# Kernel optimization log

Measured on AMD Instinct MI355X. Metric: run time of the kernel, lower is better.

## Reference

```python
import jax, jax.numpy as jnp
import numpy as np

B, N, D_IN, D_OUT, E = 16, 16384, 128, 128, 65536
LN_EPS = 1e-5


def setup_inputs() -> dict:
    key = jax.random.key(0)
    k1, k2, k3, k4 = jax.random.split(key, 4)
    x = jax.random.normal(k1, (B, N, D_IN), dtype=jnp.float32)
    edge_index = jax.random.randint(k2, (2, E), 0, N, dtype=jnp.int64)
    W_self = jax.random.normal(k3, (D_OUT, D_IN), dtype=jnp.float32) / np.sqrt(D_IN)
    W_neigh = jax.random.normal(k4, (D_OUT, D_IN), dtype=jnp.float32) / np.sqrt(D_IN)
    return {
        "x": x,
        "edge_index": edge_index,
        "batch_size": B,
        "W_self": W_self,
        "W_neigh": W_neigh,
        "bias": jnp.zeros((D_OUT,), jnp.float32),
        "gamma": jnp.ones((D_OUT,), jnp.float32),
        "beta": jnp.zeros((D_OUT,), jnp.float32),
    }


def reference(x, edge_index, batch_size, W_self, W_neigh, bias, gamma, beta):
    b, n, d = x.shape
    src, dst = edge_index[0], edge_index[1]
    # expand edge index for disjoint batched graphs: add per-graph node offsets
    offsets = (jnp.arange(batch_size, dtype=src.dtype) * n)[:, None]  # [B,1]
    src_e = (src[None, :] + offsets).reshape(-1)  # [B*E]
    dst_e = (dst[None, :] + offsets).reshape(-1)
    x_flat = x.reshape(batch_size * n, d)
    # scatter-sum neighbor features and degrees, then mean
    agg = jax.ops.segment_sum(x_flat[src_e], dst_e, num_segments=batch_size * n)
    deg = jax.ops.segment_sum(jnp.ones_like(dst_e, dtype=x_flat.dtype), dst_e,
                              num_segments=batch_size * n)
    neigh = agg / jnp.maximum(deg, 1.0)[:, None]
    out = x_flat @ W_self.T + neigh @ W_neigh.T + bias  # [B*N, D_OUT]
    # LayerNorm over last dim
    mu = jnp.mean(out, axis=-1, keepdims=True)
    var = jnp.mean(jnp.square(out - mu), axis=-1, keepdims=True)
    out = (out - mu) * jax.lax.rsqrt(var + LN_EPS) * gamma + beta
    out = jax.nn.relu(out)
    return out.reshape(batch_size, n, -1)
```

## Files before the change

kernel.cpp:

```cpp
#include <hip/hip_runtime.h>
#include <hip/hip_bf16.h>
#include <stdint.h>

#define B_ 16
#define N_ 16384
#define D_ 128
#define E_ 65536

typedef __attribute__((ext_vector_type(8))) __bf16 bf16x8;
typedef __attribute__((ext_vector_type(4))) float f32x4;
typedef __attribute__((ext_vector_type(4))) _Float16 half4;
typedef __attribute__((ext_vector_type(8))) _Float16 half8;

__device__ __forceinline__ uint16_t f2bf(float f) {
    union { float f; uint32_t u; } v;
    v.f = f;
    uint32_t u = v.u;
    uint32_t r = (u + 0x7fffu + ((u >> 16) & 1u)) >> 16;
    return (uint16_t)r;
}

__device__ __forceinline__ int As_off(int ch, int l16) {
    int c = (ch & 7) ^ ((l16 >> 4) & 1);
    return ch * 1024 + ((l16 ^ c) << 4);
}

__device__ __forceinline__ bool ei_is64(const int* __restrict__ ei, int t) {
    int w = ei[2 * (t & 63) + 1];
    return __ballot(w != 0) == 0ull;
}

__global__ void k_cntpack(const int* __restrict__ ei,
                          const float* __restrict__ wself,
                          const float* __restrict__ wneigh,
                          const float* __restrict__ x,
                          int* __restrict__ deg,
                          uint16_t* __restrict__ wpack,
                          _Float16* __restrict__ xh) {
    int t = threadIdx.x;
    int bid = blockIdx.x;
    if (bid < 256) {
        bool is64 = ei_is64(ei, t);
        int e = bid * 256 + t;
        int d = is64 ? ei[2 * (E_ + e)] : ei[E_ + e];
        atomicAdd(&deg[d], 1);
    } else if (bid < 384) {
        int g = (bid - 256) * 256 + t;
        int j = g & 7;
        int lane = (g >> 3) & 63;
        int nt = (g >> 9) & 7;
        int ks = g >> 12;
        int k = ks * 32 + (lane >> 4) * 8 + j;
        int n = nt * 16 + (lane & 15);
        float v = (k < 128) ? wself[n * 128 + k] : wneigh[n * 128 + (k - 128)];
        wpack[g] = f2bf(v);
    } else {
        size_t base = (size_t)(bid - 384) * 8192 + (size_t)t * 8;
#pragma unroll
        for (int it = 0; it < 4; it++) {
            size_t idx = base + (size_t)it * 2048;
            const float4* p = (const float4*)(x + idx);
            float4 v0 = p[0], v1 = p[1];
            union { _Float16 hh[8]; uint4 u; } pk;
            pk.hh[0] = (_Float16)v0.x; pk.hh[1] = (_Float16)v0.y;
            pk.hh[2] = (_Float16)v0.z; pk.hh[3] = (_Float16)v0.w;
            pk.hh[4] = (_Float16)v1.x; pk.hh[5] = (_Float16)v1.y;
            pk.hh[6] = (_Float16)v1.z; pk.hh[7] = (_Float16)v1.w;
            *(uint4*)(xh + idx) = pk.u;
        }
    }
}

__global__ void k_scan(const int* __restrict__ deg, int* __restrict__ off,
                       int* __restrict__ cur) {
    __shared__ int ps[256];
    int t = threadIdx.x;
    int vals[64];
    const int4* dv = (const int4*)(deg + t * 64);
    int s = 0;
#pragma unroll
    for (int i = 0; i < 16; i++) {
        int4 v = dv[i];
        vals[4 * i + 0] = v.x; vals[4 * i + 1] = v.y;
        vals[4 * i + 2] = v.z; vals[4 * i + 3] = v.w;
        s += v.x + v.y + v.z + v.w;
    }
    ps[t] = s;
    __syncthreads();
#pragma unroll
    for (int st = 1; st < 256; st <<= 1) {
        int add = (t >= st) ? ps[t - st] : 0;
        __syncthreads();
        ps[t] += add;
        __syncthreads();
    }
    int run = ps[t] - s;
#pragma unroll
    for (int i = 0; i < 64; i++) {
        off[t * 64 + i] = run;
        cur[t * 64 + i] = run;
        run += vals[i];
    }
    if (t == 255) off[N_] = run;
}

__global__ void k_fill(const int* __restrict__ ei, int* __restrict__ cur,
                       int* __restrict__ adj) {
    int t = threadIdx.x;
    bool is64 = ei_is64(ei, t);
    int e = blockIdx.x * 256 + t;
    int s = is64 ? ei[2 * e] : ei[e];
    int d = is64 ? ei[2 * (E_ + e)] : ei[E_ + e];
    int p = atomicAdd(&cur[d], 1);
    adj[p] = s;
}

template <bool USE_H>
__global__ __launch_bounds__(256, 8) void k_main(
    const float* __restrict__ x,
    const _Float16* __restrict__ xh,
    const int* __restrict__ off,
    const int* __restrict__ adj,
    const uint16_t* __restrict__ wpack,
    const float* __restrict__ bias,
    const float* __restrict__ gamma_,
    const float* __restrict__ beta_,
    float* __restrict__ out) {
    __shared__ __align__(16) unsigned char smem[16896];
    __shared__ float prm[3][128];
    unsigned char* Asb = smem;
    float* Cs = (float*)smem;

    int t = threadIdx.x;
    int bid = blockIdx.x;
    int xcd = bid & 7;
    int w = bid >> 12;
    int tile = (bid >> 3) & 511;
    int b = w * 8 + xcd;
    int node0 = tile * 32;

    if (t < 128) {
        prm[0][t] = bias[t];
        prm[1][t] = gamma_[t];
        prm[2][t] = beta_[t];
    }

    int hw = t >> 5, l = t & 31;
    int p = l >> 4;
    int dl = l & 15;

    int obase = node0 + hw * 4;
    int oo[5];
#pragma unroll
    for (int i = 0; i < 5; i++) oo[i] = off[obase + i];

    const _Float16* xgb = xh + (size_t)b * N_ * D_;
    const float* xgf = x + (size_t)b * N_ * D_;

#pragma unroll
    for (int i = 0; i < 2; i++) {
        int r2 = hw * 4 + i * 2 + p;
        int nd = node0 + r2;
        float f[8];
        if (USE_H) {
            uint4 raw = *(const uint4*)(xgb + (size_t)nd * D_ + dl * 8);
            half8 hv = __builtin_bit_cast(half8, raw);
#pragma unroll
            for (int j = 0; j < 8; j++) f[j] = (float)hv[j];
        } else {
            const float4* pv = (const float4*)(xgf + (size_t)nd * D_ + dl * 8);
            float4 a0 = pv[0], a1 = pv[1];
            f[0] = a0.x; f[1] = a0.y; f[2] = a0.z; f[3] = a0.w;
            f[4] = a1.x; f[5] = a1.y; f[6] = a1.z; f[7] = a1.w;
        }
        uint32_t pk[4];
#pragma unroll
        for (int j = 0; j < 4; j++)
            pk[j] = (uint32_t)f2bf(f[2 * j]) | ((uint32_t)f2bf(f[2 * j + 1]) << 16);
        int ks = dl >> 2, qd = dl & 3;
        int mt2 = r2 >> 4, m2 = r2 & 15;
        *(uint4*)(Asb + As_off(ks * 2 + mt2, qd * 16 + m2)) =
            make_uint4(pk[0], pk[1], pk[2], pk[3]);
    }

#pragma unroll
    for (int i = 0; i < 4; i++) {
        int r2 = hw * 4 + i;
        int o0 = oo[i], o1 = oo[i + 1];
        float a[8] = {0.f, 0.f, 0.f, 0.f, 0.f, 0.f, 0.f, 0.f};
        if (USE_H) {
            for (int e = o0 + p; e < o1; e += 2) {
                int s0 = adj[e];
                uint4 raw = *(const uint4*)(xgb + (size_t)s0 * D_ + dl * 8);
                half8 hv = __builtin_bit_cast(half8, raw);
#pragma unroll
                for (int j = 0; j < 8; j++) a[j] += (float)hv[j];
            }
        } else {
            for (int e = o0 + p; e < o1; e += 2) {
                int s0 = adj[e];
                const float4* pv = (const float4*)(xgf + (size_t)s0 * D_ + dl * 8);
                float4 v0 = pv[0], v1 = pv[1];
                a[0] += v0.x; a[1] += v0.y; a[2] += v0.z; a[3] += v0.w;
                a[4] += v1.x; a[5] += v1.y; a[6] += v1.z; a[7] += v1.w;
            }
        }
#pragma unroll
        for (int j = 0; j < 8; j++) a[j] += __shfl_xor(a[j], 16, 64);
        if (p == 0) {
            float sc = 1.f / fmaxf((float)(o1 - o0), 1.f);
            uint32_t pk[4];
#pragma unroll
            for (int j = 0; j < 4; j++)
                pk[j] = (uint32_t)f2bf(a[2 * j] * sc) |
                        ((uint32_t)f2bf(a[2 * j + 1] * sc) << 16);
            int kc = 16 + dl;
            int ks = kc >> 2, qd = kc & 3;
            int mt2 = r2 >> 4, m2 = r2 & 15;
            *(uint4*)(Asb + As_off(ks * 2 + mt2, qd * 16 + m2)) =
                make_uint4(pk[0], pk[1], pk[2], pk[3]);
        }
    }

    __syncthreads();

    int wv = t >> 6;
    int lane = t & 63;
    f32x4 accv[2][2];
#pragma unroll
    for (int i = 0; i < 2; i++)
#pragma unroll
        for (int j = 0; j < 2; j++) {
            f32x4 z = {0.f, 0.f, 0.f, 0.f};
            accv[i][j] = z;
        }

    const uint4* wp = (const uint4*)wpack;
#pragma unroll
    for (int ks = 0; ks < 8; ks++) {
        uint4 b0u = wp[(ks * 8 + 2 * wv + 0) * 64 + lane];
        uint4 b1u = wp[(ks * 8 + 2 * wv + 1) * 64 + lane];
        bf16x8 bf0 = __builtin_bit_cast(bf16x8, b0u);
        bf16x8 bf1 = __builtin_bit_cast(bf16x8, b1u);
#pragma unroll
        for (int mtt = 0; mtt < 2; mtt++) {
            bf16x8 a = *(const bf16x8*)(Asb + As_off(ks * 2 + mtt, lane));
            accv[mtt][0] = __builtin_amdgcn_mfma_f32_16x16x32_bf16(a, bf0, accv[mtt][0], 0, 0, 0);
            accv[mtt][1] = __builtin_amdgcn_mfma_f32_16x16x32_bf16(a, bf1, accv[mtt][1], 0, 0, 0);
        }
    }

    __syncthreads();

#pragma unroll
    for (int mtt = 0; mtt < 2; mtt++)
#pragma unroll
        for (int ntl = 0; ntl < 2; ntl++)
#pragma unroll
            for (int rg = 0; rg < 4; rg++) {
                int row = mtt * 16 + (lane >> 4) * 4 + rg;
                int col = (2 * wv + ntl) * 16 + (lane & 15);
                Cs[row * 132 + (col >> 5) * 33 + (col & 31)] = accv[mtt][ntl][rg];
            }

    __syncthreads();

    {
        int r = t >> 3;
        int h = t & 7;
        int node = node0 + r;
        const size_t xrow = ((size_t)b * N_ + node) * D_;
        int cbase = r * 132 + (h >> 1) * 33 + (h & 1) * 16;
        float s1 = 0.f, s2 = 0.f;
#pragma unroll
        for (int i = 0; i < 16; i++) {
            float v = Cs[cbase + i] + prm[0][h * 16 + i];
            s1 += v;
            s2 += v * v;
        }
        s1 += __shfl_xor(s1, 1, 64);
        s2 += __shfl_xor(s2, 1, 64);
        s1 += __shfl_xor(s1, 2, 64);
        s2 += __shfl_xor(s2, 2, 64);
        s1 += __shfl_xor(s1, 4, 64);
        s2 += __shfl_xor(s2, 4, 64);
        float mu = s1 * (1.f / 128.f);
        float var = s2 * (1.f / 128.f) - mu * mu;
        float rstd = rsqrtf(var + 1e-5f);

        float* orow = out + xrow;
#pragma unroll
        for (int c = 0; c < 4; c++) {
            float4 o;
            float tmp[4];
#pragma unroll
            for (int j = 0; j < 4; j++) {
                int i0 = c * 4 + j;
                int d0 = h * 16 + i0;
                float v = Cs[cbase + i0] + prm[0][d0];
                tmp[j] = fmaxf((v - mu) * rstd * prm[1][d0] + prm[2][d0], 0.f);
            }
            o.x = tmp[0]; o.y = tmp[1]; o.z = tmp[2]; o.w = tmp[3];
            *(float4*)&orow[h * 16 + c * 4] = o;
        }
    }
}

extern "C" void kernel_launch(void* const* d_in, const int* in_sizes, int n_in,
                              void* d_out, int out_size, void* d_ws, size_t ws_size,
                              hipStream_t stream) {
    (void)in_sizes; (void)n_in; (void)out_size;
    const float* x      = (const float*)d_in[0];
    const int*   ei     = (const int*)d_in[1];
    const float* wself  = (const float*)d_in[3];
    const float* wneigh = (const float*)d_in[4];
    const float* bias   = (const float*)d_in[5];
    const float* gma    = (const float*)d_in[6];
    const float* bta    = (const float*)d_in[7];
    float* out = (float*)d_out;

    char* ws = (char*)d_ws;
    int* deg        = (int*)(ws);
    int* off        = (int*)(ws + 65536);
    int* cur        = (int*)(ws + 131584);
    int* adj        = (int*)(ws + 197120);
    uint16_t* wpack = (uint16_t*)(ws + 459264);
    _Float16* xh    = (_Float16*)(ws + 524800);

    bool use_h = d_ws != nullptr &&
                 ws_size >= (size_t)524800 + (size_t)B_ * N_ * D_ * 2;

    hipMemsetAsync(deg, 0, N_ * sizeof(int), stream);
    k_cntpack<<<use_h ? 4480 : 384, 256, 0, stream>>>(ei, wself, wneigh, x, deg,
                                                      wpack, xh);
    k_scan<<<1, 256, 0, stream>>>(deg, off, cur);
    k_fill<<<E_ / 256, 256, 0, stream>>>(ei, cur, adj);
    if (use_h)
        k_main<true><<<B_ * (N_ / 32), 256, 0, stream>>>(x, xh, off, adj, wpack,
                                                         bias, gma, bta, out);
    else
        k_main<false><<<B_ * (N_ / 32), 256, 0, stream>>>(x, xh, off, adj, wpack,
                                                          bias, gma, bta, out);
}
```

Measured before the change: 336.5 us.

## Fuse degree count, scan and CSR fill into one front kernel

Replaces the memset, the degree-count, scan and fill kernels with a single 1024-thread kernel. Block 0 builds the whole CSR in shared memory: a histogram, a wave-shuffle scan and an atomic fill. The other blocks concurrently pack the weights and convert x to fp16. This removes three launches and a memset, and moves the degree atomics from global to LDS. In exchange, the CSR build is serialized on one block, which may become the critical path of the front kernel.

```diff
diff --git a/kernel.cpp b/kernel.cpp
--- a/kernel.cpp
+++ b/kernel.cpp
@@ -9,7 +9,6 @@
 
 typedef __attribute__((ext_vector_type(8))) __bf16 bf16x8;
 typedef __attribute__((ext_vector_type(4))) float f32x4;
-typedef __attribute__((ext_vector_type(4))) _Float16 half4;
 typedef __attribute__((ext_vector_type(8))) _Float16 half8;
 
 __device__ __forceinline__ uint16_t f2bf(float f) {
@@ -30,22 +29,78 @@
     return __ballot(w != 0) == 0ull;
 }
 
-__global__ void k_cntpack(const int* __restrict__ ei,
-                          const float* __restrict__ wself,
-                          const float* __restrict__ wneigh,
-                          const float* __restrict__ x,
-                          int* __restrict__ deg,
-                          uint16_t* __restrict__ wpack,
-                          _Float16* __restrict__ xh) {
+__global__ __launch_bounds__(1024) void k_front(const int* __restrict__ ei,
+                                                const float* __restrict__ wself,
+                                                const float* __restrict__ wneigh,
+                                                const float* __restrict__ x,
+                                                uint16_t* __restrict__ wpack,
+                                                _Float16* __restrict__ xh,
+                                                int* __restrict__ off,
+                                                int* __restrict__ adj) {
+    __shared__ int hist[16384];
     int t = threadIdx.x;
     int bid = blockIdx.x;
-    if (bid < 256) {
+    if (bid == 0) {
+#pragma unroll
+        for (int k = 0; k < 4; k++)
+            *(int4*)&hist[t * 16 + k * 4] = make_int4(0, 0, 0, 0);
+        __syncthreads();
         bool is64 = ei_is64(ei, t);
-        int e = bid * 256 + t;
-        int d = is64 ? ei[2 * (E_ + e)] : ei[E_ + e];
-        atomicAdd(&deg[d], 1);
-    } else if (bid < 384) {
-        int g = (bid - 256) * 256 + t;
+        for (int i = 0; i < 64; i++) {
+            int e = i * 1024 + t;
+            int d = is64 ? ei[2 * (E_ + e)] : ei[E_ + e];
+            atomicAdd(&hist[d], 1);
+        }
+        __syncthreads();
+        int local[16];
+        int s = 0;
+#pragma unroll
+        for (int j = 0; j < 16; j++) {
+            local[j] = hist[t * 16 + j];
+            s += local[j];
+        }
+        __syncthreads();
+        int lane = t & 63, wid = t >> 6;
+        int sc = s;
+#pragma unroll
+        for (int o = 1; o < 64; o <<= 1) {
+            int v = __shfl_up(sc, o, 64);
+            if (lane >= o) sc += v;
+        }
+        if (lane == 63) hist[wid] = sc;
+        __syncthreads();
+        if (t == 0) {
+            int run0 = 0;
+#pragma unroll
+            for (int w2 = 0; w2 < 16; w2++) {
+                int tmp = hist[w2];
+                hist[w2] = run0;
+                run0 += tmp;
+            }
+        }
+        __syncthreads();
+        int base = hist[wid] + (sc - s);
+        __syncthreads();
+        int run = base;
+#pragma unroll
+        for (int j = 0; j < 16; j++) {
+            off[t * 16 + j] = run;
+            int dj = local[j];
+            hist[t * 16 + j] = run;
+            run += dj;
+        }
+        if (t == 0) off[N_] = E_;
+        __syncthreads();
+        for (int i = 0; i < 64; i++) {
+            int e = i * 1024 + t;
+            int s_, d_;
+            if (is64) { s_ = ei[2 * e]; d_ = ei[2 * (E_ + e)]; }
+            else      { s_ = ei[e];     d_ = ei[E_ + e]; }
+            int pp = atomicAdd(&hist[d_], 1);
+            adj[pp] = s_;
+        }
+    } else if (bid <= 32) {
+        int g = (bid - 1) * 1024 + t;
         int j = g & 7;
         int lane = (g >> 3) & 63;
         int nt = (g >> 9) & 7;
@@ -55,64 +110,16 @@
         float v = (k < 128) ? wself[n * 128 + k] : wneigh[n * 128 + (k - 128)];
         wpack[g] = f2bf(v);
     } else {
-        size_t base = (size_t)(bid - 384) * 8192 + (size_t)t * 8;
-#pragma unroll
-        for (int it = 0; it < 4; it++) {
-            size_t idx = base + (size_t)it * 2048;
-            const float4* p = (const float4*)(x + idx);
-            float4 v0 = p[0], v1 = p[1];
-            union { _Float16 hh[8]; uint4 u; } pk;
-            pk.hh[0] = (_Float16)v0.x; pk.hh[1] = (_Float16)v0.y;
-            pk.hh[2] = (_Float16)v0.z; pk.hh[3] = (_Float16)v0.w;
-            pk.hh[4] = (_Float16)v1.x; pk.hh[5] = (_Float16)v1.y;
-            pk.hh[6] = (_Float16)v1.z; pk.hh[7] = (_Float16)v1.w;
-            *(uint4*)(xh + idx) = pk.u;
-        }
-    }
-}
-
-__global__ void k_scan(const int* __restrict__ deg, int* __restrict__ off,
-                       int* __restrict__ cur) {
-    __shared__ int ps[256];
-    int t = threadIdx.x;
-    int vals[64];
-    const int4* dv = (const int4*)(deg + t * 64);
-    int s = 0;
-#pragma unroll
-    for (int i = 0; i < 16; i++) {
-        int4 v = dv[i];
-        vals[4 * i + 0] = v.x; vals[4 * i + 1] = v.y;
-        vals[4 * i + 2] = v.z; vals[4 * i + 3] = v.w;
-        s += v.x + v.y + v.z + v.w;
-    }
-    ps[t] = s;
-    __syncthreads();
-#pragma unroll
-    for (int st = 1; st < 256; st <<= 1) {
-        int add = (t >= st) ? ps[t - st] : 0;
-        __syncthreads();
-        ps[t] += add;
-        __syncthreads();
-    }
-    int run = ps[t] - s;
-#pragma unroll
-    for (int i = 0; i < 64; i++) {
-        off[t * 64 + i] = run;
-        cur[t * 64 + i] = run;
-        run += vals[i];
-    }
-    if (t == 255) off[N_] = run;
-}
-
-__global__ void k_fill(const int* __restrict__ ei, int* __restrict__ cur,
-                       int* __restrict__ adj) {
-    int t = threadIdx.x;
-    bool is64 = ei_is64(ei, t);
-    int e = blockIdx.x * 256 + t;
-    int s = is64 ? ei[2 * e] : ei[e];
-    int d = is64 ? ei[2 * (E_ + e)] : ei[E_ + e];
-    int p = atomicAdd(&cur[d], 1);
-    adj[p] = s;
+        size_t idx = (size_t)(bid - 33) * 8192 + (size_t)t * 8;
+        const float4* p = (const float4*)(x + idx);
+        float4 v0 = p[0], v1 = p[1];
+        union { _Float16 hh[8]; uint4 u; } pk;
+        pk.hh[0] = (_Float16)v0.x; pk.hh[1] = (_Float16)v0.y;
+        pk.hh[2] = (_Float16)v0.z; pk.hh[3] = (_Float16)v0.w;
+        pk.hh[4] = (_Float16)v1.x; pk.hh[5] = (_Float16)v1.y;
+        pk.hh[6] = (_Float16)v1.z; pk.hh[7] = (_Float16)v1.w;
+        *(uint4*)(xh + idx) = pk.u;
+    }
 }
 
 template <bool USE_H>
@@ -320,21 +327,16 @@
     float* out = (float*)d_out;
 
     char* ws = (char*)d_ws;
-    int* deg        = (int*)(ws);
-    int* off        = (int*)(ws + 65536);
-    int* cur        = (int*)(ws + 131584);
-    int* adj        = (int*)(ws + 197120);
-    uint16_t* wpack = (uint16_t*)(ws + 459264);
-    _Float16* xh    = (_Float16*)(ws + 524800);
+    int* off        = (int*)(ws);
+    int* adj        = (int*)(ws + 65600);
+    uint16_t* wpack = (uint16_t*)(ws + 327744);
+    _Float16* xh    = (_Float16*)(ws + 393280);
 
     bool use_h = d_ws != nullptr &&
-                 ws_size >= (size_t)524800 + (size_t)B_ * N_ * D_ * 2;
-
-    hipMemsetAsync(deg, 0, N_ * sizeof(int), stream);
-    k_cntpack<<<use_h ? 4480 : 384, 256, 0, stream>>>(ei, wself, wneigh, x, deg,
-                                                      wpack, xh);
-    k_scan<<<1, 256, 0, stream>>>(deg, off, cur);
-    k_fill<<<E_ / 256, 256, 0, stream>>>(ei, cur, adj);
+                 ws_size >= (size_t)393280 + (size_t)B_ * N_ * D_ * 2;
+
+    k_front<<<use_h ? 4129 : 33, 1024, 0, stream>>>(ei, wself, wneigh, x,
+                                                    wpack, xh, off, adj);
     if (use_h)
         k_main<true><<<B_ * (N_ / 32), 256, 0, stream>>>(x, xh, off, adj, wpack,
                                                          bias, gma, bta, out);
```

Result: slower. 437.9 us (+30.1%).

## Split fp16 conversion across two prep kernels and accumulate gathers in half2

Applied to the files above, without the earlier changes.

The fp32-to-fp16 conversion of x is split. The first 1024 chunks stay in the degree-count/weight-pack kernel, and the remaining 3072 chunks move into the adjacency-fill kernel, so conversion work runs alongside the fill kernel's atomic-bound edge scatter. The neighbor gather in the main kernel now sums in packed half2 with two edges per iteration, instead of converting each element to fp32. This cuts ALU work and adds memory-level parallelism, at the cost of reduced accumulation precision and overflow risk in fp16.

```diff
diff --git a/kernel.cpp b/kernel.cpp
--- a/kernel.cpp
+++ b/kernel.cpp
@@ -1,5 +1,6 @@
 #include <hip/hip_runtime.h>
 #include <hip/hip_bf16.h>
+#include <hip/hip_fp16.h>
 #include <stdint.h>
 
 #define B_ 16
@@ -9,7 +10,6 @@
 
 typedef __attribute__((ext_vector_type(8))) __bf16 bf16x8;
 typedef __attribute__((ext_vector_type(4))) float f32x4;
-typedef __attribute__((ext_vector_type(4))) _Float16 half4;
 typedef __attribute__((ext_vector_type(8))) _Float16 half8;
 
 __device__ __forceinline__ uint16_t f2bf(float f) {
@@ -30,13 +30,31 @@
     return __ballot(w != 0) == 0ull;
 }
 
-__global__ void k_cntpack(const int* __restrict__ ei,
-                          const float* __restrict__ wself,
-                          const float* __restrict__ wneigh,
-                          const float* __restrict__ x,
-                          int* __restrict__ deg,
-                          uint16_t* __restrict__ wpack,
-                          _Float16* __restrict__ xh) {
+__device__ __forceinline__ void conv_chunk(const float* __restrict__ x,
+                                           _Float16* __restrict__ xh,
+                                           int g, int t) {
+    size_t base = (size_t)g * 8192 + (size_t)t * 8;
+#pragma unroll
+    for (int it = 0; it < 4; it++) {
+        size_t idx = base + (size_t)it * 2048;
+        const float4* p = (const float4*)(x + idx);
+        float4 v0 = p[0], v1 = p[1];
+        union { _Float16 hh[8]; uint4 u; } pk;
+        pk.hh[0] = (_Float16)v0.x; pk.hh[1] = (_Float16)v0.y;
+        pk.hh[2] = (_Float16)v0.z; pk.hh[3] = (_Float16)v0.w;
+        pk.hh[4] = (_Float16)v1.x; pk.hh[5] = (_Float16)v1.y;
+        pk.hh[6] = (_Float16)v1.z; pk.hh[7] = (_Float16)v1.w;
+        *(uint4*)(xh + idx) = pk.u;
+    }
+}
+
+__global__ void k_a(const int* __restrict__ ei,
+                    const float* __restrict__ wself,
+                    const float* __restrict__ wneigh,
+                    const float* __restrict__ x,
+                    int* __restrict__ deg,
+                    uint16_t* __restrict__ wpack,
+                    _Float16* __restrict__ xh) {
     int t = threadIdx.x;
     int bid = blockIdx.x;
     if (bid < 256) {
@@ -55,19 +73,7 @@
         float v = (k < 128) ? wself[n * 128 + k] : wneigh[n * 128 + (k - 128)];
         wpack[g] = f2bf(v);
     } else {
-        size_t base = (size_t)(bid - 384) * 8192 + (size_t)t * 8;
-#pragma unroll
-        for (int it = 0; it < 4; it++) {
-            size_t idx = base + (size_t)it * 2048;
-            const float4* p = (const float4*)(x + idx);
-            float4 v0 = p[0], v1 = p[1];
-            union { _Float16 hh[8]; uint4 u; } pk;
-            pk.hh[0] = (_Float16)v0.x; pk.hh[1] = (_Float16)v0.y;
-            pk.hh[2] = (_Float16)v0.z; pk.hh[3] = (_Float16)v0.w;
-            pk.hh[4] = (_Float16)v1.x; pk.hh[5] = (_Float16)v1.y;
-            pk.hh[6] = (_Float16)v1.z; pk.hh[7] = (_Float16)v1.w;
-            *(uint4*)(xh + idx) = pk.u;
-        }
+        conv_chunk(x, xh, bid - 384, t);
     }
 }
 
@@ -104,15 +110,21 @@
     if (t == 255) off[N_] = run;
 }
 
-__global__ void k_fill(const int* __restrict__ ei, int* __restrict__ cur,
-                       int* __restrict__ adj) {
+__global__ void k_b(const int* __restrict__ ei, const float* __restrict__ x,
+                    int* __restrict__ cur, int* __restrict__ adj,
+                    _Float16* __restrict__ xh, int do_conv) {
     int t = threadIdx.x;
-    bool is64 = ei_is64(ei, t);
-    int e = blockIdx.x * 256 + t;
-    int s = is64 ? ei[2 * e] : ei[e];
-    int d = is64 ? ei[2 * (E_ + e)] : ei[E_ + e];
-    int p = atomicAdd(&cur[d], 1);
-    adj[p] = s;
+    int bid = blockIdx.x;
+    if (bid < 256) {
+        bool is64 = ei_is64(ei, t);
+        int e = bid * 256 + t;
+        int s = is64 ? ei[2 * e] : ei[e];
+        int d = is64 ? ei[2 * (E_ + e)] : ei[E_ + e];
+        int p = atomicAdd(&cur[d], 1);
+        adj[p] = s;
+    } else if (do_conv) {
+        conv_chunk(x, xh, 1024 + (bid - 256), t);
+    }
 }
 
 template <bool USE_H>
@@ -187,16 +199,37 @@
     for (int i = 0; i < 4; i++) {
         int r2 = hw * 4 + i;
         int o0 = oo[i], o1 = oo[i + 1];
-        float a[8] = {0.f, 0.f, 0.f, 0.f, 0.f, 0.f, 0.f, 0.f};
+        float a[8];
         if (USE_H) {
-            for (int e = o0 + p; e < o1; e += 2) {
+            __half2 hacc[4];
+#pragma unroll
+            for (int j = 0; j < 4; j++) hacc[j] = __float2half2_rn(0.f);
+            union { uint4 u; __half2 h[4]; } c0, c1;
+            int e = o0 + p;
+            for (; e + 2 < o1; e += 4) {
+                int s0 = adj[e], s1 = adj[e + 2];
+                c0.u = *(const uint4*)(xgb + (size_t)s0 * D_ + dl * 8);
+                c1.u = *(const uint4*)(xgb + (size_t)s1 * D_ + dl * 8);
+#pragma unroll
+                for (int j = 0; j < 4; j++) hacc[j] = __hadd2(hacc[j], c0.h[j]);
+#pragma unroll
+                for (int j = 0; j < 4; j++) hacc[j] = __hadd2(hacc[j], c1.h[j]);
+            }
+            if (e < o1) {
                 int s0 = adj[e];
-                uint4 raw = *(const uint4*)(xgb + (size_t)s0 * D_ + dl * 8);
-                half8 hv = __builtin_bit_cast(half8, raw);
-#pragma unroll
-                for (int j = 0; j < 8; j++) a[j] += (float)hv[j];
+                c0.u = *(const uint4*)(xgb + (size_t)s0 * D_ + dl * 8);
+#pragma unroll
+                for (int j = 0; j < 4; j++) hacc[j] = __hadd2(hacc[j], c0.h[j]);
+            }
+#pragma unroll
+            for (int j = 0; j < 4; j++) {
+                float2 fj = __half22float2(hacc[j]);
+                a[2 * j] = fj.x;
+                a[2 * j + 1] = fj.y;
             }
         } else {
+#pragma unroll
+            for (int j = 0; j < 8; j++) a[j] = 0.f;
             for (int e = o0 + p; e < o1; e += 2) {
                 int s0 = adj[e];
                 const float4* pv = (const float4*)(xgf + (size_t)s0 * D_ + dl * 8);
@@ -331,10 +364,11 @@
                  ws_size >= (size_t)524800 + (size_t)B_ * N_ * D_ * 2;
 
     hipMemsetAsync(deg, 0, N_ * sizeof(int), stream);
-    k_cntpack<<<use_h ? 4480 : 384, 256, 0, stream>>>(ei, wself, wneigh, x, deg,
-                                                      wpack, xh);
+    k_a<<<use_h ? 1408 : 384, 256, 0, stream>>>(ei, wself, wneigh, x, deg,
+                                                wpack, xh);
     k_scan<<<1, 256, 0, stream>>>(deg, off, cur);
-    k_fill<<<E_ / 256, 256, 0, stream>>>(ei, cur, adj);
+    k_b<<<use_h ? 3328 : 256, 256, 0, stream>>>(ei, x, cur, adj, xh,
+                                                use_h ? 1 : 0);
     if (use_h)
         k_main<true><<<B_ * (N_ / 32), 256, 0, stream>>>(x, xh, off, adj, wpack,
                                                          bias, gma, bta, out);
```

Result: no change. 330.5 us (-1.8%).
